# Kernel tuning notes

Hardware: AMD Instinct MI355X
Metric: run time of the kernel (lower is better)

Reference implementation:

```python
import jax, jax.numpy as jnp
import numpy as np

ITERS = 3

def squash(x, axis=-1):
    norm = jnp.linalg.norm(x, axis=axis, keepdims=True)
    scale = norm ** 2 / (1 + norm ** 2) / (norm + 1e-08)
    return scale * x

def setup_inputs() -> dict:
    key = jax.random.key(0)
    kx, kw = jax.random.split(key)
    x = jax.random.normal(kx, (64, 8000, 8), dtype=jnp.float32)
    W = 0.01 * jax.random.normal(kw, (10, 8000, 16, 8), dtype=jnp.float32)
    return {"x": x, "W": W}

def reference(x, W):
    # u_hat[b,o,i,d] = W[o,i,d,e] @ x[b,i,e]
    u_hat = jnp.einsum('oide,bie->boid', W, x)  # [B, O, I, D]
    temp_u_hat = jax.lax.stop_gradient(u_hat)
    B, O, I, D = u_hat.shape
    b = jnp.zeros((B, O, I, 1), dtype=u_hat.dtype)
    v = jnp.ones((B, O, D), dtype=u_hat.dtype)
    for i in range(ITERS):
        c = jax.nn.softmax(b, axis=1)  # over out_caps
        if i < ITERS - 1:
            s = (c * temp_u_hat).sum(axis=2)       # [B, O, D]
            v = squash(s)
            # agreement: u_hat . v over dim D
            b = b + jnp.einsum('boid,bod->boi', temp_u_hat, v)[..., None]
        else:
            s = (c * u_hat).sum(axis=2)
            v = squash(s)
    return v
```

## Files before the change

### kernel.cpp

```cpp
#include <hip/hip_runtime.h>
#include <hip/hip_fp16.h>
#include <math.h>

#define IN 8000
#define OC 10
#define NUNIT 1000
#define VACC_F (64 * OC * 16)
#define PART_H (64 * OC * 16)

#define REC_B   28672
#define REC_H   14336
#define XOFF_B  20480
#define XOFF_H  10240
#define REC_TOTAL_B ((size_t)NUNIT * REC_B)

typedef __fp16 h2 __attribute__((ext_vector_type(2)));
typedef _Float16 half8 __attribute__((ext_vector_type(8)));
typedef float f32x16 __attribute__((ext_vector_type(16)));

__device__ __forceinline__ h2 asb(unsigned int v) { return __builtin_bit_cast(h2, v); }

__device__ __forceinline__ float dot2(h2 a, h2 b, float c) {
#if __has_builtin(__builtin_amdgcn_fdot2)
    return __builtin_amdgcn_fdot2(a, b, c, false);
#else
    return fmaf((float)a[0], (float)b[0], fmaf((float)a[1], (float)b[1], c));
#endif
}

__device__ __forceinline__ unsigned int pk_rn(float a, float b) {
    return __builtin_bit_cast(unsigned int, __float22half2_rn(make_float2(a, b)));
}

#define GLDS16(gp, lp) __builtin_amdgcn_global_load_lds(                      \
    (const __attribute__((address_space(1))) void*)(gp),                      \
    (__attribute__((address_space(3))) void*)(lp), 16, 0, 0)

__global__ __launch_bounds__(256) void caps_prep(
    const float* __restrict__ W, const float* __restrict__ x,
    __fp16* __restrict__ rec)
{
    const int t   = threadIdx.x;
    const int blk = blockIdx.x;
    if (blk < 1250) {
        const int gt = blk * 256 + t;
#pragma unroll
        for (int k = 0; k < 4; ++k) {
            int g  = gt + k * 320000;
            int u  = g / 1280;
            int r  = g - u * 1280;
            int il = r / 160;
            int rr = r - il * 160;
            int o  = rr >> 4;
            int d  = rr & 15;
            const float* ip = W + ((size_t)o * IN + (size_t)(u * 8 + il)) * 128 + d * 8;
            float4 f0 = *(const float4*)(ip);
            float4 f1 = *(const float4*)(ip + 4);
            uint4 pk = make_uint4(pk_rn(f0.x, f0.y), pk_rn(f0.z, f0.w),
                                  pk_rn(f1.x, f1.y), pk_rn(f1.z, f1.w));
            *(uint4*)(rec + (size_t)u * REC_H + il * 1280 + o * 128 + d * 8) = pk;
        }
    } else {
        const int u    = (blk - 1250) * 4 + (t >> 6);
        const int lane = t & 63;
#pragma unroll
        for (int il = 0; il < 8; ++il) {
            const float* ip = x + ((size_t)lane * IN + (size_t)(u * 8 + il)) * 8;
            float4 f0 = *(const float4*)(ip);
            float4 f1 = *(const float4*)(ip + 4);
            uint4 pk = make_uint4(pk_rn(f0.x, f0.y), pk_rn(f0.z, f0.w),
                                  pk_rn(f1.x, f1.y), pk_rn(f1.z, f1.w));
            *(uint4*)(rec + (size_t)u * REC_H + XOFF_H + il * 512 + lane * 8) = pk;
        }
    }
}

template<int UNIFORM>
__global__ __launch_bounds__(256, 2) void caps_pass(
    const __fp16* __restrict__ rec, const float* __restrict__ Vacc,
    __fp16* __restrict__ part)
{
    __shared__ __align__(16) unsigned char sm[2 * REC_B];
    __shared__ __align__(16) unsigned char zs[16];

    const int t    = threadIdx.x;
    const int w    = t >> 6;
    const int lane = t & 63;
    const int lo   = lane & 31;
    const int hi   = lane >> 5;
    const int bt   = w & 1;
    const int ph   = w >> 1;
    const int b    = bt * 32 + lo;

    if (t < 4) ((unsigned int*)zs)[t] = 0u;

    h2 vh[10][4];
    if (!UNIFORM) {
        const float* vp = Vacc + (size_t)b * (OC * 16);
        const float L2E = 1.44269504f;
#pragma unroll
        for (int o = 0; o < OC; ++o) {
            float4 fa = *(const float4*)(vp + o * 16 + 4 * hi);
            float4 fb = *(const float4*)(vp + o * 16 + 8 + 4 * hi);
            vh[o][0] = asb(pk_rn(fa.x * L2E, fa.y * L2E));
            vh[o][1] = asb(pk_rn(fa.z * L2E, fa.w * L2E));
            vh[o][2] = asb(pk_rn(fb.x * L2E, fb.y * L2E));
            vh[o][3] = asb(pk_rn(fb.z * L2E, fb.w * L2E));
        }
    }

    f32x16 acc[5];
#pragma unroll
    for (int op = 0; op < 5; ++op)
#pragma unroll
        for (int k = 0; k < 16; ++k) acc[op][k] = 0.f;

    f32x16 zc;
#pragma unroll
    for (int k = 0; k < 16; ++k) zc[k] = 0.f;

    const int bid  = blockIdx.x;
    const int grid = gridDim.x;

    auto issue = [&](int st, int bufi) {
        const char* g = (const char*)rec + (size_t)st * REC_B + (size_t)lane * 16;
        unsigned char* lb = sm + bufi * REC_B;
#pragma unroll
        for (int c = 0; c < 7; ++c) {
            const int q = c * 4 + w;
            GLDS16(g + q * 1024, lb + q * 1024);
        }
    };

    issue(bid, 0);
    if (bid + grid < NUNIT) issue(bid + grid, 1);
    __syncthreads();

    int cur = 0;
    for (int st = bid; st < NUNIT; st += grid) {
        const unsigned char* buf = sm + cur * REC_B;

        if (UNIFORM) {
#pragma unroll
            for (int ip = 0; ip < 2; ++ip) {
                const int il0 = ph * 4 + ip * 2;
                half8 xb = *(const half8*)(buf + XOFF_B + (il0 + hi) * 1024 + b * 16);
#pragma unroll
                for (int op = 0; op < 5; ++op) {
                    half8 av = *(const half8*)(buf + (il0 + hi) * 2560 + op * 512 + lo * 16);
                    acc[op] = __builtin_amdgcn_mfma_f32_32x32x16_f16(av, xb, acc[op], 0, 0, 0);
                }
            }
        } else {
#pragma unroll 1
            for (int u = 0; u < 4; ++u) {
                const int il = ph * 4 + u;
                const unsigned char* xaddr = (lane < 32)
                    ? (buf + XOFF_B + il * 1024 + b * 16)
                    : (const unsigned char*)zs;
                half8 xb = *(const half8*)xaddr;

                h2 uh2[5][8];
                float lgf[10];
#pragma unroll
                for (int op = 0; op < 5; ++op) {
                    half8 av = *(const half8*)(buf + il * 2560 + op * 512 + lo * 16);
                    f32x16 C = __builtin_amdgcn_mfma_f32_32x32x16_f16(av, xb, zc, 0, 0, 0);
#pragma unroll
                    for (int q = 0; q < 8; ++q)
                        uh2[op][q] = __builtin_amdgcn_cvt_pkrtz(C[2 * q], C[2 * q + 1]);
                    float l0 = 0.f, l1 = 0.f;
#pragma unroll
                    for (int qq = 0; qq < 4; ++qq) {
                        l0 = dot2(uh2[op][qq],     vh[op * 2][qq],     l0);
                        l1 = dot2(uh2[op][4 + qq], vh[op * 2 + 1][qq], l1);
                    }
                    lgf[op * 2]     = l0;
                    lgf[op * 2 + 1] = l1;
                }
#pragma unroll
                for (int pp = 0; pp < 5; ++pp) {
                    h2 lp = asb(pk_rn(lgf[2 * pp], lgf[2 * pp + 1]));
                    int ob = __shfl_xor(__builtin_bit_cast(int, lp), 32);
                    h2 s2 = lp + __builtin_bit_cast(h2, ob);
                    lgf[2 * pp]     = (float)s2[0];
                    lgf[2 * pp + 1] = (float)s2[1];
                }
                float mx = lgf[0];
#pragma unroll
                for (int o = 1; o < OC; ++o) mx = fmaxf(mx, lgf[o]);
                float pe[10];
                float se = 0.f;
#pragma unroll
                for (int o = 0; o < OC; ++o) {
                    pe[o] = __builtin_amdgcn_exp2f(lgf[o] - mx);
                    se += pe[o];
                }
                float rs = __builtin_amdgcn_rcpf(se);
                float c10[10];
#pragma unroll
                for (int o = 0; o < OC; ++o) c10[o] = pe[o] * rs;
#pragma unroll
                for (int op = 0; op < 5; ++op)
#pragma unroll
                    for (int r = 0; r < 16; ++r) {
                        float uv = (float)uh2[op][r >> 1][r & 1];
                        acc[op][r] = fmaf(c10[op * 2 + (r >> 3)], uv, acc[op][r]);
                    }
            }
        }

        const int nxt = st + 2 * grid;
        if (nxt < NUNIT) {
            __syncthreads();
            issue(nxt, cur);
            __syncthreads();
        }
        cur ^= 1;
    }

    float* red = (float*)sm;
#pragma unroll 1
    for (int phase = 0; phase < 2; ++phase) {
        __syncthreads();
        if (ph == phase) {
#pragma unroll
            for (int op = 0; op < 5; ++op)
#pragma unroll
                for (int rp = 0; rp < 8; ++rp) {
                    const int r = rp * 2;
                    const int o = op * 2 + (r >> 3);
                    const int d = (r & 3) + 8 * ((r >> 2) & 1) + 4 * hi;
                    float* p = &red[(size_t)b * 164 + o * 16 + d];
                    if (phase == 0) {
                        *(float2*)p = make_float2(acc[op][r], acc[op][r + 1]);
                    } else {
                        float2 v2 = *(const float2*)p;
                        v2.x += acc[op][r];
                        v2.y += acc[op][r + 1];
                        *(float2*)p = v2;
                    }
                }
        }
    }
    __syncthreads();
    unsigned int* dst = (unsigned int*)part;
    for (int q = t; q < PART_H / 2; q += 256) {
        int bo = q >> 3;
        int u8 = q & 7;
        int bb = bo / 10;
        int oo = bo - bb * 10;
        float2 v2 = *(const float2*)&red[(size_t)bb * 164 + oo * 16 + u8 * 2];
        dst[(size_t)(bo * grid + bid) * 8 + u8] = pk_rn(v2.x, v2.y);
    }
}

__global__ __launch_bounds__(256) void caps_reduce(
    const __fp16* __restrict__ part, float* __restrict__ Vacc,
    float* __restrict__ out, int nchunk, int mode, float scale)
{
    const int bo = blockIdx.x;
    const int t  = threadIdx.x;
    const int d2 = t & 3;
    const int s  = t >> 2;

    const unsigned int* p32 = (const unsigned int*)part + (size_t)bo * nchunk * 8;
    float4 a = make_float4(0.f, 0.f, 0.f, 0.f);
    for (int c = s; c < nchunk; c += 64) {
        uint2 v = *(const uint2*)(p32 + (size_t)c * 8 + d2 * 2);
        h2 lov = asb(v.x), hiv = asb(v.y);
        a.x += (float)lov[0]; a.y += (float)lov[1];
        a.z += (float)hiv[0]; a.w += (float)hiv[1];
    }
#pragma unroll
    for (int m = 4; m <= 32; m <<= 1) {
        a.x += __shfl_xor(a.x, m); a.y += __shfl_xor(a.y, m);
        a.z += __shfl_xor(a.z, m); a.w += __shfl_xor(a.w, m);
    }
    __shared__ float red[4][16];
    const int wv = t >> 6;
    if ((t & 63) < 4) {
        red[wv][d2 * 4 + 0] = a.x; red[wv][d2 * 4 + 1] = a.y;
        red[wv][d2 * 4 + 2] = a.z; red[wv][d2 * 4 + 3] = a.w;
    }
    __syncthreads();
    if (t < 16) {
        float sv = (red[0][t] + red[1][t] + red[2][t] + red[3][t]) * scale;
        float n2 = sv * sv;
#pragma unroll
        for (int m = 1; m < 16; m <<= 1) n2 += __shfl_xor(n2, m);
        float norm = sqrtf(n2);
        float scl  = n2 / (1.f + n2) / (norm + 1e-8f);
        float v = scl * sv;
        if (mode == 2)      out[bo * 16 + t] = v;
        else if (mode == 0) Vacc[bo * 16 + t] = v;
        else                Vacc[bo * 16 + t] += v;
    }
}

extern "C" void kernel_launch(void* const* d_in, const int* in_sizes, int n_in,
                              void* d_out, int out_size, void* d_ws, size_t ws_size,
                              hipStream_t stream) {
    const float* x = (const float*)d_in[0];
    const float* W = (const float*)d_in[1];
    float* out = (float*)d_out;

    char* ws = (char*)d_ws;
    float*  Vacc = (float*)ws;
    __fp16* rec  = (__fp16*)(ws + VACC_F * sizeof(float));
    __fp16* part = (__fp16*)(ws + VACC_F * sizeof(float) + REC_TOTAL_B);

    size_t head = VACC_F * sizeof(float) + REC_TOTAL_B;
    size_t avail = (ws_size > head) ? ws_size - head : 0;
    long slots = (long)(avail / (PART_H * sizeof(__fp16)));
    int grid = (int)((slots < 500) ? slots : 500);
    if (grid < 1) grid = 1;

    caps_prep<<<1500, 256, 0, stream>>>(W, x, rec);

    caps_pass<1><<<grid, 256, 0, stream>>>(rec, Vacc, part);
    caps_reduce<<<640, 256, 0, stream>>>(part, Vacc, out, grid, 0, 0.1f);
    caps_pass<0><<<grid, 256, 0, stream>>>(rec, Vacc, part);
    caps_reduce<<<640, 256, 0, stream>>>(part, Vacc, out, grid, 1, 1.0f);
    caps_pass<0><<<grid, 256, 0, stream>>>(rec, Vacc, part);
    caps_reduce<<<640, 256, 0, stream>>>(part, Vacc, out, grid, 2, 1.0f);
}
```

Before: 166.6 us.

## Single-buffer LDS, fp16 packed accumulators, and one unit per block

Drops the LDS double buffer in favour of a single record buffer plus reduction space, raising the launch bound to three blocks per SM. The grid grows to one block per unit, so each block loads and processes exactly one record. In the non-uniform passes the routing accumulators become packed fp16 with packed FMAs instead of fp32 FMAs, cutting registers and ALU work. The risks are lost load/compute overlap within a block, more partial slots for the reduce kernels to sum, and precision loss from fp16 accumulation and round-toward-zero coefficient conversion.

After: 186.8 us. 1.12x slower.

```diff
diff --git a/kernel.cpp b/kernel.cpp
--- a/kernel.cpp
+++ b/kernel.cpp
@@ -13,6 +13,8 @@
 #define XOFF_B  20480
 #define XOFF_H  10240
 #define REC_TOTAL_B ((size_t)NUNIT * REC_B)
+
+#define SM_BYTES 41984
 
 typedef __fp16 h2 __attribute__((ext_vector_type(2)));
 typedef _Float16 half8 __attribute__((ext_vector_type(8)));
@@ -76,11 +78,11 @@
 }
 
 template<int UNIFORM>
-__global__ __launch_bounds__(256, 2) void caps_pass(
+__global__ __launch_bounds__(256, 3) void caps_pass(
     const __fp16* __restrict__ rec, const float* __restrict__ Vacc,
     __fp16* __restrict__ part)
 {
-    __shared__ __align__(16) unsigned char sm[2 * REC_B];
+    __shared__ __align__(16) unsigned char sm[SM_BYTES];
     __shared__ __align__(16) unsigned char zs[16];
 
     const int t    = threadIdx.x;
@@ -110,10 +112,18 @@
     }
 
     f32x16 acc[5];
-#pragma unroll
-    for (int op = 0; op < 5; ++op)
-#pragma unroll
-        for (int k = 0; k < 16; ++k) acc[op][k] = 0.f;
+    h2 acch[5][8];
+    if (UNIFORM) {
+#pragma unroll
+        for (int op = 0; op < 5; ++op)
+#pragma unroll
+            for (int k = 0; k < 16; ++k) acc[op][k] = 0.f;
+    } else {
+#pragma unroll
+        for (int op = 0; op < 5; ++op)
+#pragma unroll
+            for (int q = 0; q < 8; ++q) acch[op][q] = h2{(__fp16)0.f, (__fp16)0.f};
+    }
 
     f32x16 zc;
 #pragma unroll
@@ -122,23 +132,23 @@
     const int bid  = blockIdx.x;
     const int grid = gridDim.x;
 
-    auto issue = [&](int st, int bufi) {
+    auto issue = [&](int st) {
         const char* g = (const char*)rec + (size_t)st * REC_B + (size_t)lane * 16;
-        unsigned char* lb = sm + bufi * REC_B;
 #pragma unroll
         for (int c = 0; c < 7; ++c) {
             const int q = c * 4 + w;
-            GLDS16(g + q * 1024, lb + q * 1024);
+            GLDS16(g + q * 1024, sm + q * 1024);
         }
     };
 
-    issue(bid, 0);
-    if (bid + grid < NUNIT) issue(bid + grid, 1);
-    __syncthreads();
-
-    int cur = 0;
+    bool first = true;
     for (int st = bid; st < NUNIT; st += grid) {
-        const unsigned char* buf = sm + cur * REC_B;
+        if (!first) __syncthreads();
+        issue(st);
+        __syncthreads();
+        first = false;
+
+        const unsigned char* buf = sm;
 
         if (UNIFORM) {
 #pragma unroll
@@ -197,26 +207,20 @@
                     se += pe[o];
                 }
                 float rs = __builtin_amdgcn_rcpf(se);
-                float c10[10];
-#pragma unroll
-                for (int o = 0; o < OC; ++o) c10[o] = pe[o] * rs;
-#pragma unroll
-                for (int op = 0; op < 5; ++op)
-#pragma unroll
-                    for (int r = 0; r < 16; ++r) {
-                        float uv = (float)uh2[op][r >> 1][r & 1];
-                        acc[op][r] = fmaf(c10[op * 2 + (r >> 3)], uv, acc[op][r]);
+#pragma unroll
+                for (int op = 0; op < 5; ++op) {
+                    float c0 = pe[op * 2] * rs;
+                    float c1 = pe[op * 2 + 1] * rs;
+                    h2 ch0 = __builtin_amdgcn_cvt_pkrtz(c0, c0);
+                    h2 ch1 = __builtin_amdgcn_cvt_pkrtz(c1, c1);
+#pragma unroll
+                    for (int q = 0; q < 4; ++q) {
+                        acch[op][q]     = ch0 * uh2[op][q]     + acch[op][q];
+                        acch[op][4 + q] = ch1 * uh2[op][4 + q] + acch[op][4 + q];
                     }
+                }
             }
         }
-
-        const int nxt = st + 2 * grid;
-        if (nxt < NUNIT) {
-            __syncthreads();
-            issue(nxt, cur);
-            __syncthreads();
-        }
-        cur ^= 1;
     }
 
     float* red = (float*)sm;
@@ -227,17 +231,18 @@
 #pragma unroll
             for (int op = 0; op < 5; ++op)
 #pragma unroll
-                for (int rp = 0; rp < 8; ++rp) {
-                    const int r = rp * 2;
-                    const int o = op * 2 + (r >> 3);
-                    const int d = (r & 3) + 8 * ((r >> 2) & 1) + 4 * hi;
-                    float* p = &red[(size_t)b * 164 + o * 16 + d];
+                for (int q = 0; q < 8; ++q) {
+                    const int o  = op * 2 + (q >> 2);
+                    const int d0 = 2 * (q & 1) + 8 * ((q >> 1) & 1) + 4 * hi;
+                    float e0, e1;
+                    if (UNIFORM) { e0 = acc[op][2 * q]; e1 = acc[op][2 * q + 1]; }
+                    else         { e0 = (float)acch[op][q][0]; e1 = (float)acch[op][q][1]; }
+                    float* p = &red[(size_t)b * 164 + o * 16 + d0];
                     if (phase == 0) {
-                        *(float2*)p = make_float2(acc[op][r], acc[op][r + 1]);
+                        *(float2*)p = make_float2(e0, e1);
                     } else {
                         float2 v2 = *(const float2*)p;
-                        v2.x += acc[op][r];
-                        v2.y += acc[op][r + 1];
+                        v2.x += e0; v2.y += e1;
                         *(float2*)p = v2;
                     }
                 }
@@ -313,7 +318,7 @@
     size_t head = VACC_F * sizeof(float) + REC_TOTAL_B;
     size_t avail = (ws_size > head) ? ws_size - head : 0;
     long slots = (long)(avail / (PART_H * sizeof(__fp16)));
-    int grid = (int)((slots < 500) ? slots : 500);
+    int grid = (int)((slots < NUNIT) ? slots : NUNIT);
     if (grid < 1) grid = 1;
 
     caps_prep<<<1500, 256, 0, stream>>>(W, x, rec);
```
